# Performance work log

Hardware: AMD Instinct MI355X
Metric: run time of the kernel (lower is better)

Reference implementation:

```python
import jax, jax.numpy as jnp
import numpy as np

N = 131072      # total nodes (128 graphs * 1024 nodes)
E = 1048576     # edges (avg degree 8)
IN = 256        # in_channels
H = 128         # hidden_channels (hardcoded 128 pad in source)
OUT = 64        # out_channels (dec_hid_dim)
G = 128         # num graphs == hidden_channels -> no padding branch
NPG = N // G    # nodes per graph


def setup_inputs() -> dict:
    key = jax.random.key(0)
    ks = jax.random.split(key, 32)
    def p(k, shape, fan):
        return (jax.random.normal(k, shape, jnp.float32) / np.sqrt(fan)).astype(jnp.float32)
    inp = {}
    inp["x"] = jax.random.normal(ks[0], (N, IN), jnp.float32)
    inp["edge_index"] = jax.random.randint(ks[1], (2, E), 0, N, dtype=jnp.int32)
    inp["batch"] = (jnp.arange(N, dtype=jnp.int32) // NPG).astype(jnp.int32)
    # GATConv layers: W, att_src, att_dst, bias
    inp["W1"], inp["as1"], inp["ad1"], inp["b1"] = p(ks[2], (IN, H), IN), p(ks[3], (H,), H), p(ks[4], (H,), H), jnp.zeros((H,), jnp.float32)
    inp["W2"], inp["as2"], inp["ad2"], inp["b2"] = p(ks[5], (H, H), H), p(ks[6], (H,), H), p(ks[7], (H,), H), jnp.zeros((H,), jnp.float32)
    inp["W3"], inp["as3"], inp["ad3"], inp["b3"] = p(ks[8], (H, H), H), p(ks[9], (H,), H), p(ks[10], (H,), H), jnp.zeros((H,), jnp.float32)
    # lin_news, lin0, lin1
    inp["Wn"], inp["bn"] = p(ks[11], (IN, H), IN), jnp.zeros((H,), jnp.float32)
    inp["W0"], inp["b0"] = p(ks[12], (H, H), H), jnp.zeros((H,), jnp.float32)
    inp["Wl"], inp["bl"] = p(ks[13], (2 * H, OUT), 2 * H), jnp.zeros((OUT,), jnp.float32)
    # attention_1 / attention_2: attn Linear(2H -> OUT) + v Linear(OUT -> 1, no bias)
    inp["Wa1"], inp["ba1"], inp["v1"] = p(ks[14], (2 * H, OUT), 2 * H), jnp.zeros((OUT,), jnp.float32), p(ks[15], (OUT,), OUT)
    inp["Wa2"], inp["ba2"], inp["v2"] = p(ks[16], (2 * H, OUT), 2 * H), jnp.zeros((OUT,), jnp.float32), p(ks[17], (OUT,), OUT)
    return inp


def _gat_layer(x, src, dst, W, a_src, a_dst, b):
    # single-head PyG GATConv (self-loops already appended to src/dst)
    h = x @ W                                   # [N, H]
    es = h @ a_src                              # [N]
    ed = h @ a_dst                              # [N]
    e = jax.nn.leaky_relu(es[src] + ed[dst], 0.2)   # [E+N]
    m = jax.ops.segment_max(e, dst, num_segments=N)
    ex = jnp.exp(e - m[dst])
    den = jax.ops.segment_sum(ex, dst, num_segments=N)
    alpha = ex / (den[dst] + 1e-16)
    out = jax.ops.segment_sum(alpha[:, None] * h[src], dst, num_segments=N)
    return out + b


def _bahdanau(hidden, enc, Wa, ba, v):
    # energy[i,j] = tanh([hidden_i; enc_j] @ Wa + ba) @ v   -> [B, B]
    Hdim = hidden.shape[1]
    eh = hidden @ Wa[:Hdim]        # [B, OUT]
    ee = enc @ Wa[Hdim:]           # [B, OUT]
    energy = jnp.tanh(eh[:, None, :] + ee[None, :, :] + ba)  # [B, B, OUT]
    return energy @ v              # [B, B]


def reference(x, edge_index, batch,
              W1, as1, ad1, b1, W2, as2, ad2, b2, W3, as3, ad3, b3,
              Wn, bn, W0, b0, Wl, bl, Wa1, ba1, v1, Wa2, ba2, v2):
    loops = jnp.arange(N, dtype=edge_index.dtype)
    src = jnp.concatenate([edge_index[0], loops])
    dst = jnp.concatenate([edge_index[1], loops])
    h = jax.nn.relu(_gat_layer(x, src, dst, W1, as1, ad1, b1))
    h = jax.nn.relu(_gat_layer(h, src, dst, W2, as2, ad2, b2))
    h = jax.nn.relu(_gat_layer(h, src, dst, W3, as3, ad3, b3))
    h = jax.ops.segment_max(h, batch, num_segments=G)        # global max pool [G, H]
    h = jax.nn.relu(h @ W0 + b0)
    # root node = first node index of each (sorted) graph
    root = jax.ops.segment_min(jnp.arange(N, dtype=jnp.int32), batch, num_segments=G)
    news = jax.nn.relu(x[root] @ Wn + bn)                    # [G, H]
    fused_h = _bahdanau(h, news, Wa1, ba1, v1)               # [G, G]
    fused_news = _bahdanau(news, h, Wa2, ba2, v2)            # [G, G]
    out = jnp.concatenate([fused_h, fused_news], axis=-1)    # [G, 2G] == [128, 256]
    out = out.reshape(-1, 2 * H) @ Wl + bl                   # [G, OUT]
    return jax.nn.sigmoid(out)
```

## Files before the change

kernel.cpp:

```cpp
#include <hip/hip_runtime.h>

#define N_NODES 131072
#define N_EDGES 1048576
#define TOT_EDG (N_NODES + N_EDGES)
#define G_GRAPHS 128
#define NPG 1024

typedef unsigned short u16;
typedef unsigned int u32;
typedef __attribute__((ext_vector_type(8))) short bh8;
typedef __attribute__((ext_vector_type(4))) float f4;

__device__ __forceinline__ float bcf(u32 u){ return __builtin_bit_cast(float, u); }
__device__ __forceinline__ u32 bcu(float f){ return __builtin_bit_cast(u32, f); }

__device__ __forceinline__ u16 f2b(float f){ return (u16)((bcu(f) + 0x8000u) >> 16); }
__device__ __forceinline__ u32 pk_rn(float lo, float hi){
    u32 a = bcu(lo) + 0x8000u;
    u32 b = bcu(hi) + 0x8000u;
    return __builtin_amdgcn_perm(b, a, 0x07060302u);
}

__global__ void wtrans_all(const float* __restrict__ W1, const float* __restrict__ W2,
                           const float* __restrict__ W3,
                           u16* __restrict__ Wt1, u16* __restrict__ Wt2, u16* __restrict__ Wt3){
    int b = blockIdx.x, t = threadIdx.x;
    if (b < 128){
        int idx = b*256 + t; int c = idx >> 8, k = idx & 255;
        Wt1[idx] = f2b(W1[k*128 + c]);
    } else if (b < 192){
        int idx = (b-128)*256 + t; int c = idx >> 7, k = idx & 127;
        Wt2[idx] = f2b(W2[k*128 + c]);
    } else {
        int idx = (b-192)*256 + t; int c = idx >> 7, k = idx & 127;
        Wt3[idx] = f2b(W3[k*128 + c]);
    }
}


__global__ __launch_bounds__(256) void bin_hist(const int* __restrict__ dst, int* __restrict__ hist){
    __shared__ int h[128];
    int b = blockIdx.x, t = threadIdx.x;
    if (t < 128) h[t] = 0;
    __syncthreads();
    int base = b*1024 + t;
    #pragma unroll
    for (int i = 0; i < 4; i++) atomicAdd(&h[dst[base + i*256] >> 10], 1);
    __syncthreads();
    if (t < 128) hist[b*128 + t] = h[t];
}

__global__ __launch_bounds__(256) void bin_scan(const int* __restrict__ hist,
                                                int* __restrict__ baseRel, int* __restrict__ total){
    int bk = blockIdx.x, t = threadIdx.x;
    int v[4]; int s = 0;
    #pragma unroll
    for (int i = 0; i < 4; i++){ v[i] = hist[(t*4+i)*128 + bk]; s += v[i]; }
    __shared__ int l[256];
    l[t] = s; __syncthreads();
    for (int off = 1; off < 256; off <<= 1){
        int u = (t >= off) ? l[t-off] : 0;
        __syncthreads();
        l[t] += u;
        __syncthreads();
    }
    int run = l[t] - s;
    #pragma unroll
    for (int i = 0; i < 4; i++){ baseRel[(t*4+i)*128 + bk] = run; run += v[i]; }
    if (t == 255) total[bk] = run;
}

__global__ void bucket_scan(const int* __restrict__ total, int* __restrict__ bstart,
                            int* __restrict__ brow, int* __restrict__ row_ptr){
    int t = threadIdx.x;
    __shared__ int l[128];
    int v = total[t];
    l[t] = v; __syncthreads();
    for (int off = 1; off < 128; off <<= 1){
        int u = (t >= off) ? l[t-off] : 0;
        __syncthreads();
        l[t] += u;
        __syncthreads();
    }
    int e = l[t] - v;
    bstart[t] = e;
    brow[t] = e + t*1024;
    if (t == 127) row_ptr[N_NODES] = TOT_EDG;
}

__global__ __launch_bounds__(256) void bin_scatter(const int* __restrict__ src, const int* __restrict__ dst,
                           const int* __restrict__ baseRel, const int* __restrict__ bstart,
                           uint2* __restrict__ binned){
    __shared__ int cur[128];
    __shared__ int bs[128];
    int b = blockIdx.x, t = threadIdx.x;
    if (t < 128){ cur[t] = baseRel[b*128 + t]; bs[t] = bstart[t]; }
    __syncthreads();
    #pragma unroll
    for (int i = 0; i < 4; i++){
        int e = b*1024 + i*256 + t;
        int s = src[e], d = dst[e];
        int bk = d >> 10;
        int r = atomicAdd(&cur[bk], 1);
        uint2 o; o.x = (u32)s; o.y = (u32)d;
        binned[bs[bk] + r] = o;
    }
}

__global__ __launch_bounds__(256) void bucket_csr(const uint2* __restrict__ binned,
                           const int* __restrict__ bstart, const int* __restrict__ total,
                           const int* __restrict__ brow,
                           int* __restrict__ row_ptr, int* __restrict__ colb){
    int b = blockIdx.x, t = threadIdx.x;
    __shared__ int cnt[1024];
    __shared__ int l[256];
    int ebeg = bstart[b], ecnt = total[b], rbase = brow[b];
    for (int i = t; i < 1024; i += 256) cnt[i] = 1;
    __syncthreads();
    for (int i = t; i < ecnt; i += 256){
        uint2 e = binned[ebeg + i];
        atomicAdd(&cnt[e.y & 1023], 1);
    }
    __syncthreads();
    int v0 = cnt[t*4], v1 = cnt[t*4+1], v2 = cnt[t*4+2], v3 = cnt[t*4+3];
    int s = v0+v1+v2+v3;
    l[t] = s; __syncthreads();
    for (int off = 1; off < 256; off <<= 1){
        int u = (t >= off) ? l[t-off] : 0;
        __syncthreads();
        l[t] += u;
        __syncthreads();
    }
    int excl = l[t] - s;
    int node0 = b*1024 + t*4;
    int p0 = rbase + excl;
    int p1 = p0 + v0, p2 = p1 + v1, p3 = p2 + v2;
    row_ptr[node0]   = p0; colb[p0] = node0;
    row_ptr[node0+1] = p1; colb[p1] = node0+1;
    row_ptr[node0+2] = p2; colb[p2] = node0+2;
    row_ptr[node0+3] = p3; colb[p3] = node0+3;
    __syncthreads();
    cnt[t*4] = p0+1; cnt[t*4+1] = p1+1; cnt[t*4+2] = p2+1; cnt[t*4+3] = p3+1;
    __syncthreads();
    for (int i = t; i < ecnt; i += 256){
        uint2 e = binned[ebeg + i];
        int p = atomicAdd(&cnt[e.y & 1023], 1);
        colb[p] = (int)e.x;
    }
}

template<int K, bool AF32>
__global__ __launch_bounds__(256) void gat_gemm(const void* __restrict__ A_,
                                                const u16* __restrict__ Bt,
                                                const float* __restrict__ asrc,
                                                const float* __restrict__ adst,
                                                u16* __restrict__ Hb,
                                                float* __restrict__ es, float* __restrict__ ed){
    constexpr int SA = 40;
    __shared__ u16 As[128*SA];
    __shared__ u16 Bs[128*SA];
    const int t = threadIdx.x;
    const int wave = t >> 6, lane = t & 63, quad = lane >> 4, m16 = lane & 15;
    const long rowBase = (long)blockIdx.x * 128;
    const int r = t >> 1, c0 = (t & 1) * 16;
    f4 acc[2][8] = {};

    for (int kk = 0; kk < K; kk += 32){
        if (AF32){
            const float* A = (const float*)A_;
            const float* src = A + (rowBase + r) * (long)K + kk + c0;
            float4 a0 = *(const float4*)(src+0);
            float4 a1 = *(const float4*)(src+4);
            float4 a2 = *(const float4*)(src+8);
            float4 a3 = *(const float4*)(src+12);
            uint4 v0, v1;
            v0.x = pk_rn(a0.x, a0.y); v0.y = pk_rn(a0.z, a0.w);
            v0.z = pk_rn(a1.x, a1.y); v0.w = pk_rn(a1.z, a1.w);
            v1.x = pk_rn(a2.x, a2.y); v1.y = pk_rn(a2.z, a2.w);
            v1.z = pk_rn(a3.x, a3.y); v1.w = pk_rn(a3.z, a3.w);
            *(uint4*)&As[r*SA + c0]     = v0;
            *(uint4*)&As[r*SA + c0 + 8] = v1;
        } else {
            const u16* A = (const u16*)A_;
            const u16* src = A + (rowBase + r) * (long)K + kk + c0;
            uint4 v0 = *(const uint4*)(src);
            uint4 v1 = *(const uint4*)(src + 8);
            *(uint4*)&As[r*SA + c0]     = v0;
            *(uint4*)&As[r*SA + c0 + 8] = v1;
        }
        {
            const u16* src = Bt + r * (long)K + kk + c0;
            uint4 v0 = *(const uint4*)(src);
            uint4 v1 = *(const uint4*)(src + 8);
            *(uint4*)&Bs[r*SA + c0]     = v0;
            *(uint4*)&Bs[r*SA + c0 + 8] = v1;
        }
        __syncthreads();
        bh8 af0 = *(const bh8*)&As[(wave*32      + m16)*SA + quad*8];
        bh8 af1 = *(const bh8*)&As[(wave*32 + 16 + m16)*SA + quad*8];
        #pragma unroll
        for (int ct = 0; ct < 8; ct++){
            bh8 bw = *(const bh8*)&Bs[(ct*16 + m16)*SA + quad*8];
            acc[0][ct] = __builtin_amdgcn_mfma_f32_16x16x32_bf16(bw, af0, acc[0][ct], 0,0,0);
            acc[1][ct] = __builtin_amdgcn_mfma_f32_16x16x32_bf16(bw, af1, acc[1][ct], 0,0,0);
        }
        __syncthreads();
    }
    #pragma unroll
    for (int nt2 = 0; nt2 < 2; nt2++){
        long node = rowBase + wave*32 + nt2*16 + m16;
        float ps = 0.f, pd = 0.f;
        #pragma unroll
        for (int ct = 0; ct < 8; ct++){
            f4 a = acc[nt2][ct];
            float4 av = *(const float4*)(asrc + ct*16 + quad*4);
            float4 dv = *(const float4*)(adst + ct*16 + quad*4);
            ps += a.x*av.x + a.y*av.y + a.z*av.z + a.w*av.w;
            pd += a.x*dv.x + a.y*dv.y + a.z*dv.z + a.w*dv.w;
            uint2 o;
            o.x = pk_rn(a.x, a.y);
            o.y = pk_rn(a.z, a.w);
            *(uint2*)(Hb + node*128 + ct*16 + quad*4) = o;
        }
        ps += __shfl_xor(ps, 16); ps += __shfl_xor(ps, 32);
        pd += __shfl_xor(pd, 16); pd += __shfl_xor(pd, 32);
        if (quad == 0){ es[node] = ps; ed[node] = pd; }
    }
}

__global__ __launch_bounds__(256) void gat_agg(const u16* __restrict__ Hb,
                        const float* __restrict__ es, const float* __restrict__ ed,
                        const int* __restrict__ row_ptr, const int* __restrict__ colv,
                        const float* __restrict__ bias, u16* __restrict__ Xb){
    int t = threadIdx.x, wave = t >> 6, lane = t & 63;
    int grp = lane >> 4, cl = lane & 15;
    int n = blockIdx.x * 4 + wave;
    int beg = row_ptr[n], end = row_ptr[n+1];
    float edn = ed[n];
    float den = 0.f;
    float a[8] = {};
    int j = beg + grp;
    for (; j + 4 < end; j += 8){
        int s0 = colv[j], s1 = colv[j+4];
        float q0 = es[s0] + edn, q1 = es[s1] + edn;
        uint4 h0 = *(const uint4*)(Hb + (long)s0*128 + cl*8);
        uint4 h1 = *(const uint4*)(Hb + (long)s1*128 + cl*8);
        q0 = fmaxf(q0, 0.f) + 0.2f*fminf(q0, 0.f);
        q1 = fmaxf(q1, 0.f) + 0.2f*fminf(q1, 0.f);
        float x0 = __expf(q0), x1 = __expf(q1);
        den += x0 + x1;
        a[0] += x0*bcf(h0.x << 16) + x1*bcf(h1.x << 16);
        a[1] += x0*bcf(h0.x & 0xffff0000u) + x1*bcf(h1.x & 0xffff0000u);
        a[2] += x0*bcf(h0.y << 16) + x1*bcf(h1.y << 16);
        a[3] += x0*bcf(h0.y & 0xffff0000u) + x1*bcf(h1.y & 0xffff0000u);
        a[4] += x0*bcf(h0.z << 16) + x1*bcf(h1.z << 16);
        a[5] += x0*bcf(h0.z & 0xffff0000u) + x1*bcf(h1.z & 0xffff0000u);
        a[6] += x0*bcf(h0.w << 16) + x1*bcf(h1.w << 16);
        a[7] += x0*bcf(h0.w & 0xffff0000u) + x1*bcf(h1.w & 0xffff0000u);
    }
    if (j < end){
        int s = colv[j];
        float e = es[s] + edn;
        e = fmaxf(e, 0.f) + 0.2f*fminf(e, 0.f);
        float ex = __expf(e);
        uint4 hv = *(const uint4*)(Hb + (long)s*128 + cl*8);
        den += ex;
        a[0] += ex * bcf(hv.x << 16);  a[1] += ex * bcf(hv.x & 0xffff0000u);
        a[2] += ex * bcf(hv.y << 16);  a[3] += ex * bcf(hv.y & 0xffff0000u);
        a[4] += ex * bcf(hv.z << 16);  a[5] += ex * bcf(hv.z & 0xffff0000u);
        a[6] += ex * bcf(hv.w << 16);  a[7] += ex * bcf(hv.w & 0xffff0000u);
    }
    #pragma unroll
    for (int k = 0; k < 8; k++){
        a[k] += __shfl_xor(a[k], 16);
        a[k] += __shfl_xor(a[k], 32);
    }
    den += __shfl_xor(den, 16); den += __shfl_xor(den, 32);
    if (grp == 0){
        float inv = 1.0f / (den + 1e-16f);
        float4 b0 = *(const float4*)(bias + cl*8);
        float4 b1 = *(const float4*)(bias + cl*8 + 4);
        uint4 ov;
        ov.x = pk_rn(fmaxf(a[0]*inv + b0.x, 0.f), fmaxf(a[1]*inv + b0.y, 0.f));
        ov.y = pk_rn(fmaxf(a[2]*inv + b0.z, 0.f), fmaxf(a[3]*inv + b0.w, 0.f));
        ov.z = pk_rn(fmaxf(a[4]*inv + b1.x, 0.f), fmaxf(a[5]*inv + b1.y, 0.f));
        ov.w = pk_rn(fmaxf(a[6]*inv + b1.z, 0.f), fmaxf(a[7]*inv + b1.w, 0.f));
        *(uint4*)(Xb + (long)n*128 + cl*8) = ov;
    }
}

__global__ void pool_part(const u16* __restrict__ Xb, float* __restrict__ pooled8){
    int b = blockIdx.x;
    int t = threadIdx.x;
    int wave = t >> 6, lane = t & 63, grp = lane >> 4, cl = lane & 15;
    long base = (long)b * 128;
    float m[8] = {};
    for (int i = 0; i < 8; i++){
        long node = base + wave*32 + i*4 + grp;
        uint4 hv = *(const uint4*)(Xb + node*128 + cl*8);
        m[0] = fmaxf(m[0], bcf(hv.x << 16));  m[1] = fmaxf(m[1], bcf(hv.x & 0xffff0000u));
        m[2] = fmaxf(m[2], bcf(hv.y << 16));  m[3] = fmaxf(m[3], bcf(hv.y & 0xffff0000u));
        m[4] = fmaxf(m[4], bcf(hv.z << 16));  m[5] = fmaxf(m[5], bcf(hv.z & 0xffff0000u));
        m[6] = fmaxf(m[6], bcf(hv.w << 16));  m[7] = fmaxf(m[7], bcf(hv.w & 0xffff0000u));
    }
    #pragma unroll
    for (int k = 0; k < 8; k++){
        m[k] = fmaxf(m[k], __shfl_xor(m[k], 16));
        m[k] = fmaxf(m[k], __shfl_xor(m[k], 32));
    }
    __shared__ float red[4][128];
    if (grp == 0){
        #pragma unroll
        for (int k = 0; k < 8; k++) red[wave][cl*8 + k] = m[k];
    }
    __syncthreads();
    if (t < 128){
        float v = fmaxf(fmaxf(red[0][t], red[1][t]), fmaxf(red[2][t], red[3][t]));
        pooled8[(long)b*128 + t] = v;
    }
}

__global__ void tail2(const float* __restrict__ x, const float* __restrict__ pooled8,
                      const float* __restrict__ Wn, const float* __restrict__ bn,
                      const float* __restrict__ W0, const float* __restrict__ b0,
                      const float* __restrict__ Wa1, const float* __restrict__ Wa2,
                      float* eh1, float* ee1, float* eh2, float* ee2){
    int g = blockIdx.x, c = threadIdx.x;
    __shared__ float xr[256], pr[128], nr[128], hr[128];
    const float* xroot = x + (size_t)g * NPG * 256;
    xr[c] = xroot[c]; xr[c+128] = xroot[c+128];
    {
        const float* pg = pooled8 + (long)g*8*128 + c;
        float v = pg[0];
        for (int s2 = 1; s2 < 8; s2++) v = fmaxf(v, pg[s2*128]);
        pr[c] = v;
    }
    __syncthreads();
    float a = bn[c];
    for (int k = 0; k < 256; k++) a += xr[k] * Wn[k*128 + c];
    a = fmaxf(a, 0.f);
    float b = b0[c];
    for (int k = 0; k < 128; k++) b += pr[k] * W0[k*128 + c];
    b = fmaxf(b, 0.f);
    nr[c] = a; hr[c] = b;
    __syncthreads();
    if (c < 64){
        int o = c; float s1 = 0.f, s2 = 0.f;
        for (int k = 0; k < 128; k++){ s1 += hr[k]*Wa1[k*64 + o]; s2 += nr[k]*Wa2[k*64 + o]; }
        eh1[g*64 + o] = s1; eh2[g*64 + o] = s2;
    } else {
        int o = c - 64; float s1 = 0.f, s2 = 0.f;
        for (int k = 0; k < 128; k++){ s1 += nr[k]*Wa1[(128+k)*64 + o]; s2 += hr[k]*Wa2[(128+k)*64 + o]; }
        ee1[g*64 + o] = s1; ee2[g*64 + o] = s2;
    }
}

__global__ void tail3(const float* __restrict__ eh1, const float* __restrict__ ee1,
                      const float* __restrict__ eh2, const float* __restrict__ ee2,
                      const float* __restrict__ ba1, const float* __restrict__ v1,
                      const float* __restrict__ ba2, const float* __restrict__ v2,
                      const float* __restrict__ Wl, const float* __restrict__ bl,
                      float* out){
    int i = blockIdx.x, t = threadIdx.x;
    __shared__ float e1i[64], e2i[64], fh[128], fn[128];
    if (t < 64) e1i[t] = eh1[i*64 + t];
    else if (t < 128) e2i[t-64] = eh2[i*64 + (t-64)];
    __syncthreads();
    if (t < 128){
        int j = t; float s = 0.f;
        for (int o = 0; o < 64; o++) s += tanhf(e1i[o] + ee1[j*64+o] + ba1[o]) * v1[o];
        fh[j] = s;
    } else {
        int j = t - 128; float s = 0.f;
        for (int o = 0; o < 64; o++) s += tanhf(e2i[o] + ee2[j*64+o] + ba2[o]) * v2[o];
        fn[j] = s;
    }
    __syncthreads();
    if (t < 64){
        int o = t; float s = bl[o];
        for (int j = 0; j < 128; j++) s += fh[j]*Wl[j*64+o] + fn[j]*Wl[(128+j)*64+o];
        out[i*64 + o] = 1.0f / (1.0f + expf(-s));
    }
}

extern "C" void kernel_launch(void* const* d_in, const int* in_sizes, int n_in,
                              void* d_out, int out_size, void* d_ws, size_t ws_size,
                              hipStream_t stream){
    const float* x   = (const float*)d_in[0];
    const int* eidx  = (const int*)d_in[1];
    const int* esrc  = eidx;
    const int* edst  = eidx + N_EDGES;
    const float* W1  = (const float*)d_in[3];
    const float* as1 = (const float*)d_in[4];
    const float* ad1 = (const float*)d_in[5];
    const float* b1  = (const float*)d_in[6];
    const float* W2  = (const float*)d_in[7];
    const float* as2 = (const float*)d_in[8];
    const float* ad2 = (const float*)d_in[9];
    const float* b2  = (const float*)d_in[10];
    const float* W3  = (const float*)d_in[11];
    const float* as3 = (const float*)d_in[12];
    const float* ad3 = (const float*)d_in[13];
    const float* b3  = (const float*)d_in[14];
    const float* Wn  = (const float*)d_in[15];
    const float* bn  = (const float*)d_in[16];
    const float* W0  = (const float*)d_in[17];
    const float* b0  = (const float*)d_in[18];
    const float* Wl  = (const float*)d_in[19];
    const float* bl  = (const float*)d_in[20];
    const float* Wa1 = (const float*)d_in[21];
    const float* ba1 = (const float*)d_in[22];
    const float* v1  = (const float*)d_in[23];
    const float* Wa2 = (const float*)d_in[24];
    const float* ba2 = (const float*)d_in[25];
    const float* v2  = (const float*)d_in[26];
    float* out = (float*)d_out;

    char* p = (char*)d_ws;
    auto take = [&](size_t b)->char*{ char* q = p; p += (b + 255) & ~(size_t)255; return q; };
    u16* Hb      = (u16*)take((size_t)N_NODES*128*2);
    u16* Xb      = (u16*)take((size_t)N_NODES*128*2);
    float* es    = (float*)take((size_t)N_NODES*4);
    float* ed    = (float*)take((size_t)N_NODES*4);
    int* row_ptr = (int*)take((size_t)(N_NODES+1)*4);
    int* colb    = (int*)take((size_t)TOT_EDG*4);
    uint2* binned= (uint2*)take((size_t)N_EDGES*8);
    int* hist    = (int*)take((size_t)1024*128*4);
    int* baseRel = (int*)take((size_t)1024*128*4);
    int* total   = (int*)take(128*4);
    int* bstart  = (int*)take(128*4);
    int* brow    = (int*)take(128*4);
    u16* Wt1     = (u16*)take(128*256*2);
    u16* Wt2     = (u16*)take(128*128*2);
    u16* Wt3     = (u16*)take(128*128*2);
    float* pooled8=(float*)take((size_t)1024*128*4);
    float* eh1   = (float*)take(128*64*4);
    float* ee1   = (float*)take(128*64*4);
    float* eh2   = (float*)take(128*64*4);
    float* ee2   = (float*)take(128*64*4);

    wtrans_all<<<256, 256, 0, stream>>>(W1, W2, W3, Wt1, Wt2, Wt3);

    bin_hist<<<1024, 256, 0, stream>>>(edst, hist);
    bin_scan<<<128, 256, 0, stream>>>(hist, baseRel, total);
    bucket_scan<<<1, 128, 0, stream>>>(total, bstart, brow, row_ptr);
    bin_scatter<<<1024, 256, 0, stream>>>(esrc, edst, baseRel, bstart, binned);
    bucket_csr<<<128, 256, 0, stream>>>(binned, bstart, total, brow, row_ptr, colb);

    gat_gemm<256, true><<<N_NODES/128, 256, 0, stream>>>(x, Wt1, as1, ad1, Hb, es, ed);
    gat_agg<<<N_NODES/4, 256, 0, stream>>>(Hb, es, ed, row_ptr, colb, b1, Xb);
    gat_gemm<128, false><<<N_NODES/128, 256, 0, stream>>>(Xb, Wt2, as2, ad2, Hb, es, ed);
    gat_agg<<<N_NODES/4, 256, 0, stream>>>(Hb, es, ed, row_ptr, colb, b2, Xb);
    gat_gemm<128, false><<<N_NODES/128, 256, 0, stream>>>(Xb, Wt3, as3, ad3, Hb, es, ed);
    gat_agg<<<N_NODES/4, 256, 0, stream>>>(Hb, es, ed, row_ptr, colb, b3, Xb);

    pool_part<<<1024, 256, 0, stream>>>(Xb, pooled8);
    tail2<<<G_GRAPHS, 128, 0, stream>>>(x, pooled8, Wn, bn, W0, b0, Wa1, Wa2, eh1, ee1, eh2, ee2);
    tail3<<<G_GRAPHS, 256, 0, stream>>>(eh1, ee1, eh2, ee2, ba1, v1, ba2, v2, Wl, bl, out);
}
```

Before: 577.0 us.

## Restructure GAT GEMM with LDS-resident weights, fuse hist into wtrans, unroll aggregation

The GEMM now stages the full 128-column weight block in LDS per 128-wide K chunk and loads each wave's 16 node rows directly from global into registers. This removes the per-32-K LDS staging of A and the extra barriers, at the cost of 64-node blocks and more LDS. The weight-transpose and edge-histogram kernels are merged into one launch to save a launch. The aggregation loop is unrolled to three edges per lane group to expose more memory-level parallelism.

Result: slower. 597.9 us (+3.6%).

```diff
diff --git a/kernel.cpp b/kernel.cpp
--- a/kernel.cpp
+++ b/kernel.cpp
@@ -21,9 +21,10 @@
     return __builtin_amdgcn_perm(b, a, 0x07060302u);
 }
 
-__global__ void wtrans_all(const float* __restrict__ W1, const float* __restrict__ W2,
+__global__ __launch_bounds__(256) void wtrans_hist(const float* __restrict__ W1, const float* __restrict__ W2,
                            const float* __restrict__ W3,
-                           u16* __restrict__ Wt1, u16* __restrict__ Wt2, u16* __restrict__ Wt3){
+                           u16* __restrict__ Wt1, u16* __restrict__ Wt2, u16* __restrict__ Wt3,
+                           const int* __restrict__ dst, int* __restrict__ hist){
     int b = blockIdx.x, t = threadIdx.x;
     if (b < 128){
         int idx = b*256 + t; int c = idx >> 8, k = idx & 255;
@@ -31,23 +32,20 @@
     } else if (b < 192){
         int idx = (b-128)*256 + t; int c = idx >> 7, k = idx & 127;
         Wt2[idx] = f2b(W2[k*128 + c]);
-    } else {
+    } else if (b < 256){
         int idx = (b-192)*256 + t; int c = idx >> 7, k = idx & 127;
         Wt3[idx] = f2b(W3[k*128 + c]);
-    }
-}
-
-
-__global__ __launch_bounds__(256) void bin_hist(const int* __restrict__ dst, int* __restrict__ hist){
-    __shared__ int h[128];
-    int b = blockIdx.x, t = threadIdx.x;
-    if (t < 128) h[t] = 0;
-    __syncthreads();
-    int base = b*1024 + t;
-    #pragma unroll
-    for (int i = 0; i < 4; i++) atomicAdd(&h[dst[base + i*256] >> 10], 1);
-    __syncthreads();
-    if (t < 128) hist[b*128 + t] = h[t];
+    } else {
+        __shared__ int h[128];
+        int bb = b - 256;
+        if (t < 128) h[t] = 0;
+        __syncthreads();
+        int base = bb*1024 + t;
+        #pragma unroll
+        for (int i = 0; i < 4; i++) atomicAdd(&h[dst[base + i*256] >> 10], 1);
+        __syncthreads();
+        if (t < 128) hist[bb*128 + t] = h[t];
+    }
 }
 
 __global__ __launch_bounds__(256) void bin_scan(const int* __restrict__ hist,
@@ -151,81 +149,74 @@
 
 template<int K, bool AF32>
 __global__ __launch_bounds__(256) void gat_gemm(const void* __restrict__ A_,
-                                                const u16* __restrict__ Bt,
+                                                const u16* __restrict__ Wt,
                                                 const float* __restrict__ asrc,
                                                 const float* __restrict__ adst,
                                                 u16* __restrict__ Hb,
                                                 float* __restrict__ es, float* __restrict__ ed){
-    constexpr int SA = 40;
-    __shared__ u16 As[128*SA];
-    __shared__ u16 Bs[128*SA];
+    constexpr int SW = 136;
+    __shared__ u16 w[128*SW];
     const int t = threadIdx.x;
     const int wave = t >> 6, lane = t & 63, quad = lane >> 4, m16 = lane & 15;
-    const long rowBase = (long)blockIdx.x * 128;
-    const int r = t >> 1, c0 = (t & 1) * 16;
-    f4 acc[2][8] = {};
-
-    for (int kk = 0; kk < K; kk += 32){
+    const long node = (long)blockIdx.x * 64 + wave*16 + m16;
+    f4 acc[8] = {};
+
+    for (int chunk = 0; chunk < K; chunk += 128){
+        if (chunk) __syncthreads();
+        {
+            int r = t >> 1;
+            int half = (t & 1) << 6;
+            const u16* src = Wt + (long)r*K + chunk + half;
+            u16* dl = &w[r*SW + half];
+            #pragma unroll
+            for (int i = 0; i < 8; i++)
+                *(uint4*)(dl + i*8) = *(const uint4*)(src + i*8);
+        }
+        __syncthreads();
+
+        bh8 bf[4];
         if (AF32){
-            const float* A = (const float*)A_;
-            const float* src = A + (rowBase + r) * (long)K + kk + c0;
-            float4 a0 = *(const float4*)(src+0);
-            float4 a1 = *(const float4*)(src+4);
-            float4 a2 = *(const float4*)(src+8);
-            float4 a3 = *(const float4*)(src+12);
-            uint4 v0, v1;
-            v0.x = pk_rn(a0.x, a0.y); v0.y = pk_rn(a0.z, a0.w);
-            v0.z = pk_rn(a1.x, a1.y); v0.w = pk_rn(a1.z, a1.w);
-            v1.x = pk_rn(a2.x, a2.y); v1.y = pk_rn(a2.z, a2.w);
-            v1.z = pk_rn(a3.x, a3.y); v1.w = pk_rn(a3.z, a3.w);
-            *(uint4*)&As[r*SA + c0]     = v0;
-            *(uint4*)&As[r*SA + c0 + 8] = v1;
+            const float* A = (const float*)A_ + node*(long)K + chunk;
+            #pragma unroll
+            for (int ks = 0; ks < 4; ks++){
+                float4 f0 = *(const float4*)(A + ks*32 + quad*8);
+                float4 f1 = *(const float4*)(A + ks*32 + quad*8 + 4);
+                uint4 uv;
+                uv.x = pk_rn(f0.x, f0.y); uv.y = pk_rn(f0.z, f0.w);
+                uv.z = pk_rn(f1.x, f1.y); uv.w = pk_rn(f1.z, f1.w);
+                bf[ks] = __builtin_bit_cast(bh8, uv);
+            }
         } else {
-            const u16* A = (const u16*)A_;
-            const u16* src = A + (rowBase + r) * (long)K + kk + c0;
-            uint4 v0 = *(const uint4*)(src);
-            uint4 v1 = *(const uint4*)(src + 8);
-            *(uint4*)&As[r*SA + c0]     = v0;
-            *(uint4*)&As[r*SA + c0 + 8] = v1;
+            const u16* A = (const u16*)A_ + node*(long)K + chunk;
+            #pragma unroll
+            for (int ks = 0; ks < 4; ks++)
+                bf[ks] = *(const bh8*)(A + ks*32 + quad*8);
         }
-        {
-            const u16* src = Bt + r * (long)K + kk + c0;
-            uint4 v0 = *(const uint4*)(src);
-            uint4 v1 = *(const uint4*)(src + 8);
-            *(uint4*)&Bs[r*SA + c0]     = v0;
-            *(uint4*)&Bs[r*SA + c0 + 8] = v1;
+        #pragma unroll
+        for (int tl = 0; tl < 8; tl++){
+            #pragma unroll
+            for (int ks = 0; ks < 4; ks++){
+                bh8 af = *(const bh8*)&w[(tl*16 + m16)*SW + ks*32 + quad*8];
+                acc[tl] = __builtin_amdgcn_mfma_f32_16x16x32_bf16(af, bf[ks], acc[tl], 0,0,0);
+            }
         }
-        __syncthreads();
-        bh8 af0 = *(const bh8*)&As[(wave*32      + m16)*SA + quad*8];
-        bh8 af1 = *(const bh8*)&As[(wave*32 + 16 + m16)*SA + quad*8];
-        #pragma unroll
-        for (int ct = 0; ct < 8; ct++){
-            bh8 bw = *(const bh8*)&Bs[(ct*16 + m16)*SA + quad*8];
-            acc[0][ct] = __builtin_amdgcn_mfma_f32_16x16x32_bf16(bw, af0, acc[0][ct], 0,0,0);
-            acc[1][ct] = __builtin_amdgcn_mfma_f32_16x16x32_bf16(bw, af1, acc[1][ct], 0,0,0);
-        }
-        __syncthreads();
-    }
-    #pragma unroll
-    for (int nt2 = 0; nt2 < 2; nt2++){
-        long node = rowBase + wave*32 + nt2*16 + m16;
-        float ps = 0.f, pd = 0.f;
-        #pragma unroll
-        for (int ct = 0; ct < 8; ct++){
-            f4 a = acc[nt2][ct];
-            float4 av = *(const float4*)(asrc + ct*16 + quad*4);
-            float4 dv = *(const float4*)(adst + ct*16 + quad*4);
-            ps += a.x*av.x + a.y*av.y + a.z*av.z + a.w*av.w;
-            pd += a.x*dv.x + a.y*dv.y + a.z*dv.z + a.w*dv.w;
-            uint2 o;
-            o.x = pk_rn(a.x, a.y);
-            o.y = pk_rn(a.z, a.w);
-            *(uint2*)(Hb + node*128 + ct*16 + quad*4) = o;
-        }
-        ps += __shfl_xor(ps, 16); ps += __shfl_xor(ps, 32);
-        pd += __shfl_xor(pd, 16); pd += __shfl_xor(pd, 32);
-        if (quad == 0){ es[node] = ps; ed[node] = pd; }
-    }
+    }
+    float ps = 0.f, pd = 0.f;
+    #pragma unroll
+    for (int tl = 0; tl < 8; tl++){
+        f4 a = acc[tl];
+        float4 av = *(const float4*)(asrc + tl*16 + quad*4);
+        float4 dv = *(const float4*)(adst + tl*16 + quad*4);
+        ps += a.x*av.x + a.y*av.y + a.z*av.z + a.w*av.w;
+        pd += a.x*dv.x + a.y*dv.y + a.z*dv.z + a.w*dv.w;
+        uint2 o;
+        o.x = pk_rn(a.x, a.y);
+        o.y = pk_rn(a.z, a.w);
+        *(uint2*)(Hb + node*128 + tl*16 + quad*4) = o;
+    }
+    ps += __shfl_xor(ps, 16); ps += __shfl_xor(ps, 32);
+    pd += __shfl_xor(pd, 16); pd += __shfl_xor(pd, 32);
+    if (quad == 0){ es[node] = ps; ed[node] = pd; }
 }
 
 __global__ __launch_bounds__(256) void gat_agg(const u16* __restrict__ Hb,
@@ -240,7 +231,27 @@
     float den = 0.f;
     float a[8] = {};
     int j = beg + grp;
-    for (; j + 4 < end; j += 8){
+    for (; j + 8 < end; j += 12){
+        int s0 = colv[j], s1 = colv[j+4], s2 = colv[j+8];
+        float q0 = es[s0] + edn, q1 = es[s1] + edn, q2 = es[s2] + edn;
+        uint4 h0 = *(const uint4*)(Hb + (long)s0*128 + cl*8);
+        uint4 h1 = *(const uint4*)(Hb + (long)s1*128 + cl*8);
+        uint4 h2 = *(const uint4*)(Hb + (long)s2*128 + cl*8);
+        q0 = fmaxf(q0, 0.f) + 0.2f*fminf(q0, 0.f);
+        q1 = fmaxf(q1, 0.f) + 0.2f*fminf(q1, 0.f);
+        q2 = fmaxf(q2, 0.f) + 0.2f*fminf(q2, 0.f);
+        float x0 = __expf(q0), x1 = __expf(q1), x2 = __expf(q2);
+        den += x0 + x1 + x2;
+        a[0] += x0*bcf(h0.x << 16) + x1*bcf(h1.x << 16) + x2*bcf(h2.x << 16);
+        a[1] += x0*bcf(h0.x & 0xffff0000u) + x1*bcf(h1.x & 0xffff0000u) + x2*bcf(h2.x & 0xffff0000u);
+        a[2] += x0*bcf(h0.y << 16) + x1*bcf(h1.y << 16) + x2*bcf(h2.y << 16);
+        a[3] += x0*bcf(h0.y & 0xffff0000u) + x1*bcf(h1.y & 0xffff0000u) + x2*bcf(h2.y & 0xffff0000u);
+        a[4] += x0*bcf(h0.z << 16) + x1*bcf(h1.z << 16) + x2*bcf(h2.z << 16);
+        a[5] += x0*bcf(h0.z & 0xffff0000u) + x1*bcf(h1.z & 0xffff0000u) + x2*bcf(h2.z & 0xffff0000u);
+        a[6] += x0*bcf(h0.w << 16) + x1*bcf(h1.w << 16) + x2*bcf(h2.w << 16);
+        a[7] += x0*bcf(h0.w & 0xffff0000u) + x1*bcf(h1.w & 0xffff0000u) + x2*bcf(h2.w & 0xffff0000u);
+    }
+    if (j + 4 < end){
         int s0 = colv[j], s1 = colv[j+4];
         float q0 = es[s0] + edn, q1 = es[s1] + edn;
         uint4 h0 = *(const uint4*)(Hb + (long)s0*128 + cl*8);
@@ -257,8 +268,7 @@
         a[5] += x0*bcf(h0.z & 0xffff0000u) + x1*bcf(h1.z & 0xffff0000u);
         a[6] += x0*bcf(h0.w << 16) + x1*bcf(h1.w << 16);
         a[7] += x0*bcf(h0.w & 0xffff0000u) + x1*bcf(h1.w & 0xffff0000u);
-    }
-    if (j < end){
+    } else if (j < end){
         int s = colv[j];
         float e = es[s] + edn;
         e = fmaxf(e, 0.f) + 0.2f*fminf(e, 0.f);
@@ -439,19 +449,18 @@
     float* eh2   = (float*)take(128*64*4);
     float* ee2   = (float*)take(128*64*4);
 
-    wtrans_all<<<256, 256, 0, stream>>>(W1, W2, W3, Wt1, Wt2, Wt3);
-
-    bin_hist<<<1024, 256, 0, stream>>>(edst, hist);
+    wtrans_hist<<<1280, 256, 0, stream>>>(W1, W2, W3, Wt1, Wt2, Wt3, edst, hist);
+
     bin_scan<<<128, 256, 0, stream>>>(hist, baseRel, total);
     bucket_scan<<<1, 128, 0, stream>>>(total, bstart, brow, row_ptr);
     bin_scatter<<<1024, 256, 0, stream>>>(esrc, edst, baseRel, bstart, binned);
     bucket_csr<<<128, 256, 0, stream>>>(binned, bstart, total, brow, row_ptr, colb);
 
-    gat_gemm<256, true><<<N_NODES/128, 256, 0, stream>>>(x, Wt1, as1, ad1, Hb, es, ed);
+    gat_gemm<256, true><<<N_NODES/64, 256, 0, stream>>>(x, Wt1, as1, ad1, Hb, es, ed);
     gat_agg<<<N_NODES/4, 256, 0, stream>>>(Hb, es, ed, row_ptr, colb, b1, Xb);
-    gat_gemm<128, false><<<N_NODES/128, 256, 0, stream>>>(Xb, Wt2, as2, ad2, Hb, es, ed);
+    gat_gemm<128, false><<<N_NODES/64, 256, 0, stream>>>(Xb, Wt2, as2, ad2, Hb, es, ed);
     gat_agg<<<N_NODES/4, 256, 0, stream>>>(Hb, es, ed, row_ptr, colb, b2, Xb);
-    gat_gemm<128, false><<<N_NODES/128, 256, 0, stream>>>(Xb, Wt3, as3, ad3, Hb, es, ed);
+    gat_gemm<128, false><<<N_NODES/64, 256, 0, stream>>>(Xb, Wt3, as3, ad3, Hb, es, ed);
     gat_agg<<<N_NODES/4, 256, 0, stream>>>(Hb, es, ed, row_ptr, colb, b3, Xb);
 
     pool_part<<<1024, 256, 0, stream>>>(Xb, pooled8);
```
